# Kernel optimization log

Measured on AMD Instinct MI355X. Metric: run time of the kernel, lower is better.

## Reference

```python
import jax, jax.numpy as jnp
import numpy as np

D = 64      # embedding_dim
GD = 8      # ground_dim
NV = 8192   # num variables (batch_size=1 * max_variables)
NC = 32768  # num clauses


def setup_inputs() -> dict:
    key = jax.random.key(0)
    ks = jax.random.split(key, 24)
    s = 1.0 / np.sqrt(D)
    sg = 1.0 / np.sqrt(GD + D)
    lin = lambda k, shp, sc: (jax.random.uniform(k, shp, jnp.float32) * 2 - 1) * sc
    inp = {
        'variables': jax.random.normal(ks[0], (1, NV, D), jnp.float32),
        'ground_vars': jax.random.normal(ks[1], (NV, GD), jnp.float32),
        # sparse 0/1 incidence matrices stored densely (as the torch code does)
        'cmat_pos': jax.random.bernoulli(ks[2], 0.02, (NC, NV)).astype(jnp.float32),
        'cmat_neg': jax.random.bernoulli(ks[3], 0.02, (NC, NV)).astype(jnp.float32),
        'v_mat': jnp.zeros((1,), jnp.float32),   # overwritten in forward; dummy
        'c_mat': jnp.zeros((1,), jnp.float32),   # overwritten in forward; dummy
        # parameters
        'fb_block': jax.random.normal(ks[4], (2, D, D), jnp.float32),  # nn_init.normal_
        'vb': jax.random.normal(ks[5], (D,), jnp.float32),
        'cb': jax.random.normal(ks[6], (D,), jnp.float32),
        # ground combiner: Linear(GD + D -> D) followed by tanh
        'Wg': lin(ks[7], (D, GD + D), sg), 'bg': lin(ks[8], (D,), sg),
        # GRU operator weights (W_*: no bias, U_*: with bias since gru_bias=True)
        'Wz': lin(ks[9], (D, D), s), 'Uz': lin(ks[10], (D, D), s), 'bz': lin(ks[11], (D,), s),
        'Wr': lin(ks[12], (D, D), s), 'Ur': lin(ks[13], (D, D), s), 'br': lin(ks[14], (D,), s),
        'Wh': lin(ks[15], (D, D), s), 'Uh': lin(ks[16], (D, D), s), 'bh': lin(ks[17], (D,), s),
    }
    return inp


def reference(variables, ground_vars, cmat_pos, cmat_neg, v_mat, c_mat,
              fb_block, vb, cb, Wg, bg, Wz, Uz, bz, Wr, Ur, br, Wh, Uh, bh):
    d = variables.shape[-1]
    v = variables.reshape(-1, d)                      # [NV, D]
    cm = cmat_pos - cmat_neg                          # signed incidence [NC, NV]
    # variable -> clause message: mm(fb[0], v.T).T == v @ fb[0].T
    vars_fwd = v @ fb_block[0].T                      # [NV, D]
    c = jax.nn.relu(cm @ vars_fwd + cb)               # [NC, D]
    # clause -> variable message via transposed incidence
    nv = cm.T @ (c @ fb_block[1].T)                   # [NV, D]
    v_emb = jax.nn.relu(nv + vb)
    # ground combiner: tanh(Linear(concat([ground, emb])))
    v_emb = jnp.tanh(jnp.concatenate([ground_vars, v_emb], axis=-1) @ Wg.T + bg)
    # GRU update against previous embeddings
    prev = v
    z = jax.nn.sigmoid(v_emb @ Wz.T + prev @ Uz.T + bz)
    r = jax.nn.sigmoid(v_emb @ Wr.T + prev @ Ur.T + br)
    h_tilda = jnp.tanh(v_emb @ Wh.T + (r * prev) @ Uh.T + bh)
    new_vars = (1 - z) * prev + z * h_tilda           # [NV, D]
    return new_vars.reshape(1, NV * d, 1)             # rc view
```

## Files before the change

### kernel.cpp

```cpp
#include <hip/hip_runtime.h>
#include <stdint.h>

typedef unsigned long long u64;

#define NVAR 8192
#define NCLS 32768
#define CSEG 16
#define GSEG 4
#define LCAP 1152

__device__ __forceinline__ float lane_bc(float v, int l) { return __shfl(v, l); }

__device__ __forceinline__ u64 readfl64(u64 x) {
  unsigned lo = __builtin_amdgcn_readfirstlane((unsigned)x);
  unsigned hi = __builtin_amdgcn_readfirstlane((unsigned)(x >> 32));
  return ((u64)hi << 32) | (u64)lo;
}

__device__ __forceinline__ u64 shflx64(u64 x, int m) {
  unsigned lo = (unsigned)__shfl_xor((int)(unsigned)x, m, 64);
  unsigned hi = (unsigned)__shfl_xor((int)(unsigned)(x >> 32), m, 64);
  return ((u64)hi << 32) | (u64)lo;
}

__global__ __launch_bounds__(256) void k_varsfwd(const float* __restrict__ v,
                                                 const float* __restrict__ fb0,
                                                 float* __restrict__ out) {
  __shared__ float fbt[64 * 64];
  __shared__ float vrow[4][64];
  int t = threadIdx.x;
#pragma unroll
  for (int i = 0; i < 16; ++i) {
    int idx = i * 256 + t;
    fbt[(idx & 63) * 64 + (idx >> 6)] = fb0[idx];
  }
  __syncthreads();
  int w = t >> 6, lane = t & 63;
  for (int rr = 0; rr < 16; rr += 4) {
    int row = blockIdx.x * 16 + rr + w;
    vrow[w][lane] = v[row * 64 + lane];
    __syncthreads();
    double a = 0.0;
#pragma unroll
    for (int k = 0; k < 64; ++k)
      a = fma((double)vrow[w][k], (double)fbt[k * 64 + lane], a);
    out[row * 64 + lane] = (float)a;
    __syncthreads();
  }
}

__global__ __launch_bounds__(512, 8) void k_pass1v3(
    const float* __restrict__ pos, const float* __restrict__ neg,
    const float* __restrict__ vfwd, const float* __restrict__ fb1,
    const float* __restrict__ cbias, float* __restrict__ dmat,
    u64* __restrict__ vbs) {
  __shared__ float sbuf[128 * 64];
  __shared__ u64 lm[2][32][4];
  __shared__ u64 lsg[2][32][4];
  int t = threadIdx.x;
  int w = __builtin_amdgcn_readfirstlane(t >> 6);
  int lane = t & 63;
  int bx = blockIdx.x;
  int c0 = bx * 32;
  int cb = bx >> 1;
  int h = bx & 1;
  double acc[4];
#pragma unroll
  for (int i = 0; i < 4; ++i) acc[i] = 0.0;

  for (int g = 0; g < 32; ++g) {
    int par = g & 1;
    const float4* s0 = (const float4*)(vfwd + (size_t)g * 256 * 64);
    float4 st0 = s0[t], st1 = s0[t + 512], st2 = s0[t + 1024], st3 = s0[t + 1536];
#pragma unroll
    for (int i = 0; i < 4; i += 2) {
      size_t rb0 = (size_t)(c0 + w * 4 + i) * 2048 + (size_t)g * 64 + lane;
      size_t rb1 = rb0 + 2048;
      float4 p0 = ((const float4*)pos)[rb0];
      float4 q0 = ((const float4*)neg)[rb0];
      float4 p1 = ((const float4*)pos)[rb1];
      float4 q1 = ((const float4*)neg)[rb1];
      float a0[4], a1[4];
      a0[0] = p0.x - q0.x; a0[1] = p0.y - q0.y; a0[2] = p0.z - q0.z; a0[3] = p0.w - q0.w;
      a1[0] = p1.x - q1.x; a1[1] = p1.y - q1.y; a1[2] = p1.z - q1.z; a1[3] = p1.w - q1.w;
      int cl0 = w * 4 + i, cl1 = cl0 + 1;
#pragma unroll
      for (int j = 0; j < 4; ++j) {
        u64 m = __ballot(a0[j] != 0.f);
        u64 sg = __ballot(a0[j] < 0.f);
        if (lane == j) { lm[par][cl0][j] = m; lsg[par][cl0][j] = sg; }
      }
#pragma unroll
      for (int j = 0; j < 4; ++j) {
        u64 m = __ballot(a1[j] != 0.f);
        u64 sg = __ballot(a1[j] < 0.f);
        if (lane == j) { lm[par][cl1][j] = m; lsg[par][cl1][j] = sg; }
      }
    }
    __syncthreads();

    {
      float4* dst = (float4*)sbuf;
      dst[t] = st0; dst[t + 512] = st1; dst[t + 1024] = st2; dst[t + 1536] = st3;
    }
    if (w < 4) {
      int jw = w;
      u64 A = (lane < 32) ? lm[par][lane][jw] : lsg[par][lane - 32][jw];
#define BSTEP(J, M)                                          \
      {                                                      \
        u64 B = shflx64(A, J);                               \
        u64 keep = (lane & J) ? ~(u64)(M) : (u64)(M);        \
        u64 B2 = (lane & J) ? (B >> J) : (B << J);           \
        A = (A & keep) | (B2 & ~keep);                       \
      }
      BSTEP(32, 0x00000000FFFFFFFFULL)
      BSTEP(16, 0x0000FFFF0000FFFFULL)
      BSTEP(8,  0x00FF00FF00FF00FFULL)
      BSTEP(4,  0x0F0F0F0F0F0F0F0FULL)
      BSTEP(2,  0x3333333333333333ULL)
      BSTEP(1,  0x5555555555555555ULL)
#undef BSTEP
      int v = (g << 8) + (lane << 2) + jw;
      vbs[((size_t)v * 512 + cb) * 2 + h] = A;
    }
    __syncthreads();

    const float4* s1 = s0 + 2048;
    st0 = s1[t]; st1 = s1[t + 512]; st2 = s1[t + 1024]; st3 = s1[t + 1536];
#pragma unroll
    for (int i = 0; i < 4; ++i) {
      int cl = w * 4 + i;
#pragma unroll
      for (int j = 0; j < 4; ++j) {
        u64 m = readfl64(lm[par][cl][j]) & 0xffffffffULL;
        u64 sg = readfl64(lsg[par][cl][j]);
        while (m) {
          int l = __builtin_ctzll(m);
          m &= m - 1;
          float dv = sbuf[(l * 4 + j) * 64 + lane];
          acc[i] += ((sg >> l) & 1) ? -(double)dv : (double)dv;
        }
      }
    }
    __syncthreads();

    {
      float4* dst = (float4*)sbuf;
      dst[t] = st0; dst[t + 512] = st1; dst[t + 1024] = st2; dst[t + 1536] = st3;
    }
    __syncthreads();

#pragma unroll
    for (int i = 0; i < 4; ++i) {
      int cl = w * 4 + i;
#pragma unroll
      for (int j = 0; j < 4; ++j) {
        u64 m = readfl64(lm[par][cl][j]) >> 32;
        u64 sg = readfl64(lsg[par][cl][j]) >> 32;
        while (m) {
          int l = __builtin_ctzll(m);
          m &= m - 1;
          float dv = sbuf[(l * 4 + j) * 64 + lane];
          acc[i] += ((sg >> l) & 1) ? -(double)dv : (double)dv;
        }
      }
    }
  }
  __syncthreads();

#pragma unroll
  for (int i2 = 0; i2 < 8; ++i2) {
    int idx = i2 * 512 + t;
    sbuf[(idx & 63) * 64 + (idx >> 6)] = fb1[idx];
  }
  float* crow = sbuf + 4096 + w * 64;
  __syncthreads();
  for (int i = 0; i < 4; ++i) {
    float cv = fmaxf((float)acc[i] + cbias[lane], 0.f);
    crow[lane] = cv;
    __syncthreads();
    double da = 0.0;
#pragma unroll
    for (int k = 0; k < 64; ++k)
      da = fma((double)crow[k], (double)sbuf[k * 64 + lane], da);
    dmat[(size_t)(c0 + w * 4 + i) * 64 + lane] = (float)da;
    __syncthreads();
  }
}

__global__ __launch_bounds__(256, 8) void k_gather4(const u64* __restrict__ vbs,
                                                    const float* __restrict__ dmat,
                                                    double* __restrict__ nvd) {
  __shared__ unsigned short list[4][LCAP];
  int w = __builtin_amdgcn_readfirstlane(threadIdx.x >> 6);
  int lane = threadIdx.x & 63;
  int seg = blockIdx.x >> 11;
  int v = (blockIdx.x & 2047) * 4 + w;
  int cc0 = seg * (512 / GSEG);
  const u64* P = vbs + ((size_t)v * 512 + cc0) * 2;
  u64 a0 = P[lane * 4 + 0], a1 = P[lane * 4 + 1];
  u64 b0 = P[lane * 4 + 2], b1 = P[lane * 4 + 3];
  u64 m0 = (a0 & 0xffffffffULL) | (a1 << 32);
  u64 s0 = (a0 >> 32) | (a1 & 0xffffffff00000000ULL);
  u64 m1 = (b0 & 0xffffffffULL) | (b1 << 32);
  u64 s1 = (b0 >> 32) | (b1 & 0xffffffff00000000ULL);
  int cnt = __popcll(m0) + __popcll(m1);
  int pre = cnt;
#pragma unroll
  for (int d = 1; d < 64; d <<= 1) {
    int o = __shfl_up(pre, d, 64);
    if (lane >= d) pre += o;
  }
  int tot = __shfl(pre, 63, 64);
  int base = pre - cnt;
#pragma unroll
  for (int half = 0; half < 2; ++half) {
    u64 m = half ? m1 : m0;
    u64 s = half ? s1 : s0;
    int cbase = (cc0 + 2 * lane + half) * 64;
    while (m) {
      int b = __builtin_ctzll(m);
      m &= m - 1;
      if (base < LCAP)
        list[w][base] = (unsigned short)((cbase + b) | (((s >> b) & 1) << 15));
      ++base;
    }
  }
  __syncthreads();
  if (tot > LCAP) tot = LCAP;
  const u64* lp = (const u64*)&list[w][0];
  double acc = 0.0;
  int k = 0;
  for (; k + 8 <= tot; k += 8) {
    u64 L0 = lp[k >> 2], L1 = lp[(k >> 2) + 1];
    unsigned e[8];
#pragma unroll
    for (int q = 0; q < 4; ++q) {
      e[q] = (unsigned)(L0 >> (16 * q)) & 0xffffu;
      e[4 + q] = (unsigned)(L1 >> (16 * q)) & 0xffffu;
    }
    float dv[8];
#pragma unroll
    for (int q = 0; q < 8; ++q)
      dv[q] = dmat[(size_t)(e[q] & 0x7fffu) * 64 + lane];
#pragma unroll
    for (int q = 0; q < 8; ++q)
      acc += (e[q] & 0x8000u) ? -(double)dv[q] : (double)dv[q];
  }
  for (; k < tot; ++k) {
    unsigned e = list[w][k];
    float dv = dmat[(size_t)(e & 0x7fffu) * 64 + lane];
    acc += (e & 0x8000u) ? -(double)dv : (double)dv;
  }
  atomicAdd(&nvd[(size_t)v * 64 + lane], acc);
}

__global__ __launch_bounds__(256) void k_pass1_basic(
    const float* __restrict__ pos, const float* __restrict__ neg,
    const float* __restrict__ bmat, const float* __restrict__ fb1,
    const float* __restrict__ cbias, float* __restrict__ dmat) {
  __shared__ float fbt[64 * 64];
  __shared__ float crow[4][64];
  int t = threadIdx.x;
#pragma unroll
  for (int i = 0; i < 16; ++i) {
    int idx = i * 256 + t;
    fbt[(idx & 63) * 64 + (idx >> 6)] = fb1[idx];
  }
  __syncthreads();
  int w = t >> 6, lane = t & 63;
  int c = blockIdx.x * 4 + w;
  const float4* prow = (const float4*)(pos + (size_t)c * NVAR);
  const float4* nrow = (const float4*)(neg + (size_t)c * NVAR);
  double acc = 0.0;
  for (int g = 0; g < 32; ++g) {
    float4 p = prow[g * 64 + lane];
    float4 q = nrow[g * 64 + lane];
    float sc[4];
    sc[0] = p.x - q.x; sc[1] = p.y - q.y; sc[2] = p.z - q.z; sc[3] = p.w - q.w;
#pragma unroll
    for (int j = 0; j < 4; ++j) {
      float s = sc[j];
      u64 m = __ballot(s != 0.f);
      u64 sg = __ballot(s < 0.f);
      while (m) {
        int l = __builtin_ctzll(m);
        m &= m - 1;
        float dv = bmat[(size_t)((g << 8) + (l << 2) + j) * 64 + lane];
        acc += ((sg >> l) & 1) ? -(double)dv : (double)dv;
      }
    }
  }
  float cv = fmaxf((float)acc + cbias[lane], 0.f);
  crow[w][lane] = cv;
  __syncthreads();
  double da = 0.0;
#pragma unroll
  for (int k = 0; k < 64; ++k)
    da = fma((double)crow[w][k], (double)fbt[k * 64 + lane], da);
  dmat[(size_t)c * 64 + lane] = (float)da;
}

__global__ __launch_bounds__(256) void k_pass2_dense(
    const float* __restrict__ pos, const float* __restrict__ neg,
    const float* __restrict__ dmat, double* __restrict__ nvd) {
  __shared__ float acc[64 * 64];
  int t = threadIdx.x;
#pragma unroll
  for (int i = 0; i < 16; ++i) acc[i * 256 + t] = 0.f;
  __syncthreads();
  int w = t >> 6, lane = t & 63;
  int s = blockIdx.x / CSEG, seg = blockIdx.x % CSEG;
  int c0 = seg * (NCLS / CSEG);
  for (int c = c0 + w; c < c0 + NCLS / CSEG; c += 4) {
    float p = pos[(size_t)c * NVAR + (s << 6) + lane];
    float q = neg[(size_t)c * NVAR + (s << 6) + lane];
    float sv = p - q;
    u64 m = __ballot(sv != 0.f);
    if (!m) continue;
    float dv = dmat[(size_t)c * 64 + lane];
    while (m) {
      int l = __builtin_ctzll(m);
      m &= m - 1;
      float sl = lane_bc(sv, l);
      atomicAdd(&acc[(l << 6) + lane], sl * dv);
    }
  }
  __syncthreads();
  size_t obase = (size_t)s * 4096;
#pragma unroll
  for (int i = 0; i < 16; ++i) {
    int idx = i * 256 + t;
    atomicAdd(&nvd[obase + idx], (double)acc[idx]);
  }
}

__global__ __launch_bounds__(256, 1) void k_tailfused(
    const double* __restrict__ nvd, const float* __restrict__ vb,
    const float* __restrict__ ground, const float* __restrict__ Wg,
    const float* __restrict__ bg,
    const float* __restrict__ Wz, const float* __restrict__ Uz,
    const float* __restrict__ bz,
    const float* __restrict__ Wr, const float* __restrict__ Ur,
    const float* __restrict__ br,
    const float* __restrict__ Wh, const float* __restrict__ Uh,
    const float* __restrict__ bh,
    const float* __restrict__ prev, float* __restrict__ out) {
  __shared__ float wg[72 * 65];
  __shared__ float wz[64 * 65], uz[64 * 65], wr[64 * 65], ur[64 * 65],
      wh[64 * 65], uh[64 * 65];
  __shared__ float xrow[4][72], yrow[4][64], prow[4][64], rprow[4][64];
  int t = threadIdx.x;
#pragma unroll
  for (int i = 0; i < 18; ++i) {
    int idx = i * 256 + t;
    wg[(idx % 72) * 65 + (idx / 72)] = Wg[idx];
  }
#pragma unroll
  for (int i = 0; i < 16; ++i) {
    int idx = i * 256 + t;
    int a = (idx & 63) * 65 + (idx >> 6);
    wz[a] = Wz[idx]; uz[a] = Uz[idx]; wr[a] = Wr[idx];
    ur[a] = Ur[idx]; wh[a] = Wh[idx]; uh[a] = Uh[idx];
  }
  __syncthreads();
  int w = t >> 6, lane = t & 63;
  for (int rr = 0; rr < 8; ++rr) {
    int row = blockIdx.x * 32 + w * 8 + rr;
    float pv = prev[row * 64 + lane];
    float ve = fmaxf((float)nvd[row * 64 + lane] + vb[lane], 0.f);
    xrow[w][8 + lane] = ve;
    if (lane < 8) xrow[w][lane] = ground[row * 8 + lane];
    prow[w][lane] = pv;
    double a = 0.0;
#pragma unroll
    for (int k = 0; k < 72; ++k)
      a = fma((double)xrow[w][k], (double)wg[k * 65 + lane], a);
    float ve2 = tanhf((float)a + bg[lane]);
    yrow[w][lane] = ve2;
    float az = bz[lane], ar = br[lane];
#pragma unroll
    for (int k = 0; k < 64; ++k) {
      float y = yrow[w][k], p = prow[w][k];
      az = fmaf(y, wz[k * 65 + lane], az);
      az = fmaf(p, uz[k * 65 + lane], az);
      ar = fmaf(y, wr[k * 65 + lane], ar);
      ar = fmaf(p, ur[k * 65 + lane], ar);
    }
    float r = 1.f / (1.f + expf(-ar));
    rprow[w][lane] = r * pv;
    float ah = bh[lane];
#pragma unroll
    for (int k = 0; k < 64; ++k) {
      ah = fmaf(yrow[w][k], wh[k * 65 + lane], ah);
      ah = fmaf(rprow[w][k], uh[k * 65 + lane], ah);
    }
    float z = 1.f / (1.f + expf(-az));
    float hh = tanhf(ah);
    out[row * 64 + lane] = (1.f - z) * pv + z * hh;
  }
}

extern "C" void kernel_launch(void* const* d_in, const int* in_sizes, int n_in,
                              void* d_out, int out_size, void* d_ws, size_t ws_size,
                              hipStream_t stream) {
  const float* variables = (const float*)d_in[0];
  const float* ground    = (const float*)d_in[1];
  const float* cpos      = (const float*)d_in[2];
  const float* cneg      = (const float*)d_in[3];
  const float* fb        = (const float*)d_in[6];
  const float* vb        = (const float*)d_in[7];
  const float* cb        = (const float*)d_in[8];
  const float* Wg        = (const float*)d_in[9];
  const float* bg        = (const float*)d_in[10];
  const float* Wz        = (const float*)d_in[11];
  const float* Uz        = (const float*)d_in[12];
  const float* bz        = (const float*)d_in[13];
  const float* Wr        = (const float*)d_in[14];
  const float* Ur        = (const float*)d_in[15];
  const float* br        = (const float*)d_in[16];
  const float* Wh        = (const float*)d_in[17];
  const float* Uh        = (const float*)d_in[18];
  const float* bh        = (const float*)d_in[19];
  float* out = (float*)d_out;
  char* ws = (char*)d_ws;
  const size_t MB = (size_t)1 << 20;

  float* vfwd   = (float*)(ws + 0);
  float* dmat   = (float*)(ws + 2 * MB);
  double* nvd   = (double*)(ws + 10 * MB);
  u64* vbs      = (u64*)(ws + 16 * MB);
  bool fast = ws_size >= 80 * MB;

  k_varsfwd<<<512, 256, 0, stream>>>(variables, fb, vfwd);
  hipMemsetAsync(nvd, 0, (size_t)NVAR * 64 * sizeof(double), stream);
  if (fast) {
    k_pass1v3<<<1024, 512, 0, stream>>>(cpos, cneg, vfwd, fb + 4096, cb, dmat,
                                        vbs);
    k_gather4<<<2048 * GSEG, 256, 0, stream>>>(vbs, dmat, nvd);
  } else {
    k_pass1_basic<<<8192, 256, 0, stream>>>(cpos, cneg, vfwd, fb + 4096, cb, dmat);
    k_pass2_dense<<<128 * CSEG, 256, 0, stream>>>(cpos, cneg, dmat, nvd);
  }
  k_tailfused<<<256, 256, 0, stream>>>(nvd, vb, ground, Wg, bg, Wz, Uz, bz,
                                       Wr, Ur, br, Wh, Uh, bh, variables, out);
}
```

Baseline: 881.6 us.

## Prefetch incidence rows a group ahead and stage vfwd via direct global-to-LDS loads

Result: slower. 1.087 ms (+23.3%).

```diff
diff --git a/kernel.cpp b/kernel.cpp
--- a/kernel.cpp
+++ b/kernel.cpp
@@ -21,6 +21,12 @@
   unsigned lo = (unsigned)__shfl_xor((int)(unsigned)x, m, 64);
   unsigned hi = (unsigned)__shfl_xor((int)(unsigned)(x >> 32), m, 64);
   return ((u64)hi << 32) | (u64)lo;
+}
+
+__device__ __forceinline__ void gload_lds16(const void* g, void* l) {
+  __builtin_amdgcn_global_load_lds(
+      (const __attribute__((address_space(1))) void*)g,
+      (__attribute__((address_space(3))) void*)l, 16, 0, 0);
 }
 
 __global__ __launch_bounds__(256) void k_varsfwd(const float* __restrict__ v,
@@ -49,14 +55,13 @@
   }
 }
 
-__global__ __launch_bounds__(512, 8) void k_pass1v3(
+__global__ __launch_bounds__(512, 8) void k_pass1v4(
     const float* __restrict__ pos, const float* __restrict__ neg,
     const float* __restrict__ vfwd, const float* __restrict__ fb1,
     const float* __restrict__ cbias, float* __restrict__ dmat,
     u64* __restrict__ vbs) {
-  __shared__ float sbuf[128 * 64];
-  __shared__ u64 lm[2][32][4];
-  __shared__ u64 lsg[2][32][4];
+  __shared__ __align__(16) float sbuf[128 * 64];
+  __shared__ __align__(16) u64 lms[2][32][4][2];
   int t = threadIdx.x;
   int w = __builtin_amdgcn_readfirstlane(t >> 6);
   int lane = t & 63;
@@ -68,44 +73,60 @@
 #pragma unroll
   for (int i = 0; i < 4; ++i) acc[i] = 0.0;
 
+  const size_t rbase = (size_t)(c0 + w * 4) * 2048 + lane;
+  float4 p0 = ((const float4*)pos)[rbase];
+  float4 q0 = ((const float4*)neg)[rbase];
+  float4 p1 = ((const float4*)pos)[rbase + 2048];
+  float4 q1 = ((const float4*)neg)[rbase + 2048];
+  float4 p2 = ((const float4*)pos)[rbase + 4096];
+  float4 q2 = ((const float4*)neg)[rbase + 4096];
+  float4 p3 = ((const float4*)pos)[rbase + 6144];
+  float4 q3 = ((const float4*)neg)[rbase + 6144];
+
   for (int g = 0; g < 32; ++g) {
     int par = g & 1;
-    const float4* s0 = (const float4*)(vfwd + (size_t)g * 256 * 64);
-    float4 st0 = s0[t], st1 = s0[t + 512], st2 = s0[t + 1024], st3 = s0[t + 1536];
-#pragma unroll
-    for (int i = 0; i < 4; i += 2) {
-      size_t rb0 = (size_t)(c0 + w * 4 + i) * 2048 + (size_t)g * 64 + lane;
-      size_t rb1 = rb0 + 2048;
-      float4 p0 = ((const float4*)pos)[rb0];
-      float4 q0 = ((const float4*)neg)[rb0];
-      float4 p1 = ((const float4*)pos)[rb1];
-      float4 q1 = ((const float4*)neg)[rb1];
-      float a0[4], a1[4];
-      a0[0] = p0.x - q0.x; a0[1] = p0.y - q0.y; a0[2] = p0.z - q0.z; a0[3] = p0.w - q0.w;
-      a1[0] = p1.x - q1.x; a1[1] = p1.y - q1.y; a1[2] = p1.z - q1.z; a1[3] = p1.w - q1.w;
-      int cl0 = w * 4 + i, cl1 = cl0 + 1;
+    auto ball = [&](float4 P, float4 Q, int cl) {
+      float sc[4] = {P.x - Q.x, P.y - Q.y, P.z - Q.z, P.w - Q.w};
 #pragma unroll
       for (int j = 0; j < 4; ++j) {
-        u64 m = __ballot(a0[j] != 0.f);
-        u64 sg = __ballot(a0[j] < 0.f);
-        if (lane == j) { lm[par][cl0][j] = m; lsg[par][cl0][j] = sg; }
+        u64 m = __ballot(sc[j] != 0.f);
+        u64 sg = __ballot(sc[j] < 0.f);
+        if (lane == j) { lms[par][cl][j][0] = m; lms[par][cl][j][1] = sg; }
       }
-#pragma unroll
-      for (int j = 0; j < 4; ++j) {
-        u64 m = __ballot(a1[j] != 0.f);
-        u64 sg = __ballot(a1[j] < 0.f);
-        if (lane == j) { lm[par][cl1][j] = m; lsg[par][cl1][j] = sg; }
-      }
-    }
-    __syncthreads();
+    };
+    ball(p0, q0, w * 4 + 0);
+    ball(p1, q1, w * 4 + 1);
+    ball(p2, q2, w * 4 + 2);
+    ball(p3, q3, w * 4 + 3);
+    asm volatile("s_waitcnt lgkmcnt(0)" ::: "memory");
+    __builtin_amdgcn_sched_barrier(0);
+    __builtin_amdgcn_s_barrier();
+    __builtin_amdgcn_sched_barrier(0);
 
     {
-      float4* dst = (float4*)sbuf;
-      dst[t] = st0; dst[t + 512] = st1; dst[t + 1024] = st2; dst[t + 1536] = st3;
-    }
+      const float* gb = vfwd + (size_t)g * 16384;
+#pragma unroll
+      for (int i = 0; i < 4; ++i)
+        gload_lds16(gb + ((size_t)(i * 512) + w * 64 + lane) * 4,
+                    (char*)sbuf + i * 8192 + w * 1024);
+    }
+    __builtin_amdgcn_sched_barrier(0);
+    {
+      int gg = (g + 1) & 31;
+      size_t rb = rbase + (size_t)gg * 64;
+      p0 = ((const float4*)pos)[rb];
+      q0 = ((const float4*)neg)[rb];
+      p1 = ((const float4*)pos)[rb + 2048];
+      q1 = ((const float4*)neg)[rb + 2048];
+      p2 = ((const float4*)pos)[rb + 4096];
+      q2 = ((const float4*)neg)[rb + 4096];
+      p3 = ((const float4*)pos)[rb + 6144];
+      q3 = ((const float4*)neg)[rb + 6144];
+    }
+    __builtin_amdgcn_sched_barrier(0);
     if (w < 4) {
       int jw = w;
-      u64 A = (lane < 32) ? lm[par][lane][jw] : lsg[par][lane - 32][jw];
+      u64 A = (lane < 32) ? lms[par][lane][jw][0] : lms[par][lane - 32][jw][1];
 #define BSTEP(J, M)                                          \
       {                                                      \
         u64 B = shflx64(A, J);                               \
@@ -122,18 +143,21 @@
 #undef BSTEP
       int v = (g << 8) + (lane << 2) + jw;
       vbs[((size_t)v * 512 + cb) * 2 + h] = A;
-    }
-    __syncthreads();
-
-    const float4* s1 = s0 + 2048;
-    st0 = s1[t]; st1 = s1[t + 512]; st2 = s1[t + 1024]; st3 = s1[t + 1536];
+      asm volatile("s_waitcnt vmcnt(9)" ::: "memory");
+    } else {
+      asm volatile("s_waitcnt vmcnt(8)" ::: "memory");
+    }
+    __builtin_amdgcn_sched_barrier(0);
+    __builtin_amdgcn_s_barrier();
+    __builtin_amdgcn_sched_barrier(0);
+
 #pragma unroll
     for (int i = 0; i < 4; ++i) {
       int cl = w * 4 + i;
 #pragma unroll
       for (int j = 0; j < 4; ++j) {
-        u64 m = readfl64(lm[par][cl][j]) & 0xffffffffULL;
-        u64 sg = readfl64(lsg[par][cl][j]);
+        u64 m = readfl64(lms[par][cl][j][0]) & 0xffffffffULL;
+        u64 sg = readfl64(lms[par][cl][j][1]);
         while (m) {
           int l = __builtin_ctzll(m);
           m &= m - 1;
@@ -142,21 +166,28 @@
         }
       }
     }
-    __syncthreads();
+    __builtin_amdgcn_s_barrier();
+    __builtin_amdgcn_sched_barrier(0);
 
     {
-      float4* dst = (float4*)sbuf;
-      dst[t] = st0; dst[t + 512] = st1; dst[t + 1024] = st2; dst[t + 1536] = st3;
-    }
-    __syncthreads();
+      const float* gb = vfwd + (size_t)g * 16384 + 8192;
+#pragma unroll
+      for (int i = 0; i < 4; ++i)
+        gload_lds16(gb + ((size_t)(i * 512) + w * 64 + lane) * 4,
+                    (char*)sbuf + i * 8192 + w * 1024);
+    }
+    asm volatile("s_waitcnt vmcnt(0)" ::: "memory");
+    __builtin_amdgcn_sched_barrier(0);
+    __builtin_amdgcn_s_barrier();
+    __builtin_amdgcn_sched_barrier(0);
 
 #pragma unroll
     for (int i = 0; i < 4; ++i) {
       int cl = w * 4 + i;
 #pragma unroll
       for (int j = 0; j < 4; ++j) {
-        u64 m = readfl64(lm[par][cl][j]) >> 32;
-        u64 sg = readfl64(lsg[par][cl][j]) >> 32;
+        u64 m = readfl64(lms[par][cl][j][0]) >> 32;
+        u64 sg = readfl64(lms[par][cl][j][1]) >> 32;
         while (m) {
           int l = __builtin_ctzll(m);
           m &= m - 1;
@@ -191,7 +222,7 @@
 __global__ __launch_bounds__(256, 8) void k_gather4(const u64* __restrict__ vbs,
                                                     const float* __restrict__ dmat,
                                                     double* __restrict__ nvd) {
-  __shared__ unsigned short list[4][LCAP];
+  __shared__ __align__(16) unsigned short list[4][LCAP];
   int w = __builtin_amdgcn_readfirstlane(threadIdx.x >> 6);
   int lane = threadIdx.x & 63;
   int seg = blockIdx.x >> 11;
@@ -435,7 +466,7 @@
   k_varsfwd<<<512, 256, 0, stream>>>(variables, fb, vfwd);
   hipMemsetAsync(nvd, 0, (size_t)NVAR * 64 * sizeof(double), stream);
   if (fast) {
-    k_pass1v3<<<1024, 512, 0, stream>>>(cpos, cneg, vfwd, fb + 4096, cb, dmat,
+    k_pass1v4<<<1024, 512, 0, stream>>>(cpos, cneg, vfwd, fb + 4096, cb, dmat,
                                         vbs);
     k_gather4<<<2048 * GSEG, 256, 0, stream>>>(vbs, dmat, nvd);
   } else {
```
